# Optimization experiments

Hardware: AMD Instinct MI355X
Metric: run time of the kernel (lower is better)

The kernel has to match this reference:

```python
import jax, jax.numpy as jnp
import numpy as np

DEPTH, DIM, HEADS, DH = 6, 1024, 16, 64
INNER = int(DIM * 2 * 4 / 3)        # 2730 (GEGLU FFN inner dim)
INNER2 = INNER * 2                  # 5460
B, N = 2, 1024
NUM_BUCKETS, MAX_DIST = 32, 128
ALPHA = 0.1                         # grad_shrink alpha (identity in fwd)


def setup_inputs() -> dict:
    key = jax.random.key(0)
    ks = jax.random.split(key, 12)
    s = 0.02
    return {
        "x": jax.random.normal(ks[0], (B, N, DIM), jnp.float32),
        "rel_emb": jax.random.normal(ks[1], (NUM_BUCKETS, HEADS), jnp.float32) * s,
        "qn_g": jnp.ones((DEPTH, DIM), jnp.float32),
        "wq": jax.random.normal(ks[2], (DEPTH, DIM, HEADS * DH), jnp.float32) * s,
        "wkv": jax.random.normal(ks[3], (DEPTH, DIM, 2 * DH), jnp.float32) * s,
        "wo": jax.random.normal(ks[4], (DEPTH, HEADS * DH, DIM), jnp.float32) * s,
        "ln1_g": jnp.ones((DEPTH, DIM), jnp.float32),
        "w1": jax.random.normal(ks[5], (DEPTH, DIM, INNER2), jnp.float32) * s,
        "convw": jax.random.normal(ks[6], (DEPTH, INNER2, 3), jnp.float32) * s,
        "ln2_g": jnp.ones((DEPTH, INNER), jnp.float32),
        "w2": jax.random.normal(ks[7], (DEPTH, INNER, DIM), jnp.float32) * s,
        "final_g": jnp.ones((DIM,), jnp.float32),
    }


def _ln(x, g):
    m = jnp.mean(x, axis=-1, keepdims=True)
    v = jnp.mean(jnp.square(x - m), axis=-1, keepdims=True)
    return (x - m) * jax.lax.rsqrt(v + 1e-5) * g


def _rel_pos_bias(rel_emb, n):
    # T5-style buckets, causal variant (as in RelativePositionBias.forward)
    q_pos = jnp.arange(n)
    k_pos = jnp.arange(n)
    npos = jnp.maximum(q_pos[:, None] - k_pos[None, :], 0)   # -relative_position, clamped
    max_exact = NUM_BUCKETS // 2
    nf = jnp.maximum(npos, 1).astype(jnp.float32)
    val_large = max_exact + (jnp.log(nf / max_exact) / np.log(MAX_DIST / max_exact)
                             * (NUM_BUCKETS - max_exact)).astype(jnp.int32)
    val_large = jnp.minimum(val_large, NUM_BUCKETS - 1)
    bucket = jnp.where(npos < max_exact, npos, val_large)
    return rel_emb[bucket].transpose(2, 0, 1)  # [h, i, j]


def _forward(x, rel_emb, qn_g, wq, wkv, wo, ln1_g, w1, convw, ln2_g, w2, final_g):
    b, n, _ = x.shape
    x = x * ALPHA + jax.lax.stop_gradient(x) * (1.0 - ALPHA)  # grad_shrink
    bias = _rel_pos_bias(rel_emb, n)                          # [h, n, n]
    causal = jnp.triu(jnp.ones((n, n), bool), 1)
    neg = -jnp.finfo(x.dtype).max
    scale = DH ** -0.5

    for l in range(DEPTH):
        # --- causal self-attention (single-head K/V) ---
        h = _ln(x, qn_g[l])
        q = (h @ wq[l]).reshape(b, n, HEADS, DH).transpose(0, 2, 1, 3) * scale  # [b,h,n,d]
        kv = h @ wkv[l]
        k, v = kv[..., :DH], kv[..., DH:]                                       # [b,n,d]
        sim = jnp.einsum('bhid,bjd->bhij', q, k) + bias
        sim = jnp.where(causal, neg, sim)
        attn = jax.nn.softmax(sim, axis=-1)
        o = jnp.einsum('bhij,bjd->bhid', attn, v)
        o = o.transpose(0, 2, 1, 3).reshape(b, n, HEADS * DH)
        x = o @ wo[l] + x

        # --- FFN: LN -> Linear -> causal depthwise conv -> GEGLU -> LN -> Linear ---
        h = _ln(x, ln1_g[l]) @ w1[l]                 # [b, n, INNER2]
        hp = jnp.pad(h, ((0, 0), (2, 0), (0, 0)))    # causal pad
        w = convw[l]                                  # [INNER2, 3]
        h = hp[:, :-2] * w[:, 0] + hp[:, 1:-1] * w[:, 1] + hp[:, 2:] * w[:, 2]
        a, gate = h[..., :INNER], h[..., INNER:]
        h = jax.nn.gelu(gate, approximate=False) * a
        h = _ln(h, ln2_g[l]) @ w2[l]
        x = h + x

    return _ln(x, final_g)


def reference(x, rel_emb, qn_g, wq, wkv, wo, ln1_g, w1, convw, ln2_g, w2, final_g):
    return _forward(x, rel_emb, qn_g, wq, wkv, wo, ln1_g, w1, convw, ln2_g, w2, final_g)
```

## Files before the change

### kernel.cpp

```cpp
#include <hip/hip_runtime.h>
#include <math.h>

#define DEPTH 6
#define DIM 1024
#define HEADS 16
#define DH 64
#define INNER 2730
#define INNER2 5460
#define INNERP 2752
#define N1P 5504
#define BATCH 2
#define SEQ 1024
#define TOK (BATCH*SEQ)
#define QKVW 1152

#define OFF_WO 1179648ull
#define OFF_W1 2228224ull
#define OFF_W2 7864320ull
#define LWT    10682368ull
#define TILES_PER_LAYER 1312

typedef unsigned short ushort;
typedef __attribute__((ext_vector_type(8))) short short8;
typedef __attribute__((ext_vector_type(4))) short short4v;
typedef __attribute__((ext_vector_type(4))) unsigned short ushort4v;
typedef __attribute__((ext_vector_type(2))) unsigned short ushort2v;
typedef __attribute__((ext_vector_type(4))) float floatx4;

__device__ inline ushort f2bf(float f) {
  unsigned int u = __float_as_uint(f);
  u += 0x7FFF + ((u >> 16) & 1);
  return (ushort)(u >> 16);
}
__device__ inline float bf2f(ushort u) {
  return __uint_as_float(((unsigned int)u) << 16);
}

__device__ inline void gload_lds16(const ushort* g, ushort* l) {
  __builtin_amdgcn_global_load_lds(
      (const __attribute__((address_space(1))) unsigned int*)g,
      (__attribute__((address_space(3))) unsigned int*)l, 16, 0, 0);
}

__global__ void bias_frag_kernel(const float* __restrict__ rel_emb, float* __restrict__ bias_c) {
  int h = blockIdx.x >> 4, dq = blockIdx.x & 15;
  for (int i = threadIdx.x; i < 4096; i += 256) {
    int reg = i & 3, col = (i >> 2) & 15, j = (i >> 6) & 3, rowgrp = i >> 8;
    int row = rowgrp * 4 + reg, colg = j * 16 + col;
    int d = dq * 64 + row - colg;
    d = d < 0 ? 0 : (d > 1023 ? 1023 : d);
    int bucket;
    if (d < 16) {
      bucket = d;
    } else {
      float nf = (float)d;
      int vl = 16 + (int)(logf(nf / 16.0f) / 2.0794415416798357f * 16.0f);
      bucket = vl < 31 ? vl : 31;
    }
    bias_c[((size_t)(h * 16 + dq)) * 4096 + i] = rel_emb[bucket * HEADS + h];
  }
}

__device__ inline void transpose_body(const float* __restrict__ W, ushort* __restrict__ Wt,
                                      int K, int N, int Kp, int Np, float scale,
                                      int k0, int n0, size_t dst_row0) {
  __shared__ float t[64][65];
  int tid = threadIdx.x;
  int kl = tid >> 4, nc = (tid & 15) * 4;
#pragma unroll
  for (int it = 0; it < 4; it++) {
    int k = kl + it * 16;
    int gk = k0 + k, gn = n0 + nc;
    floatx4 v = {0.f, 0.f, 0.f, 0.f};
    if (gk < K && gn < N) v = *(const floatx4*)&W[(size_t)gk * N + gn];
    t[nc + 0][k] = v[0] * scale;
    t[nc + 1][k] = v[1] * scale;
    t[nc + 2][k] = v[2] * scale;
    t[nc + 3][k] = v[3] * scale;
  }
  __syncthreads();
  int nr = tid >> 3, q = tid & 7;
#pragma unroll
  for (int it = 0; it < 2; it++) {
    int n = nr + it * 32;
    if (n0 + n < Np) {
      short8 p;
#pragma unroll
      for (int e = 0; e < 8; e++) p[e] = (short)f2bf(t[n][q * 8 + e]);
      *(short8*)&Wt[(dst_row0 + n) * Kp + k0 + q * 8] = p;
    }
  }
}

__global__ __launch_bounds__(256) void transpose_vec(const float* __restrict__ W,
                                                     ushort* __restrict__ Wt,
                                                     int K, int N, int Kp, int Np, float scale) {
  transpose_body(W, Wt, K, N, Kp, Np, scale, blockIdx.y * 64, blockIdx.x * 64,
                 (size_t)blockIdx.x * 64);
}

__global__ __launch_bounds__(256) void transpose_qkv(const float* __restrict__ wq,
                                                     const float* __restrict__ wkv,
                                                     ushort* __restrict__ Wt) {
  int bx = blockIdx.x;
  if (bx < 16) {
    transpose_body(wq, Wt, 1024, 1024, 1024, 1024, 0.125f, blockIdx.y * 64, bx * 64,
                   (size_t)bx * 64);
  } else {
    transpose_body(wkv, Wt, 1024, 128, 1024, 128, 1.0f, blockIdx.y * 64, (bx - 16) * 64,
                   (size_t)1024 + (bx - 16) * 64);
  }
}

__device__ inline void transpose_body128(const float* __restrict__ W, ushort* __restrict__ Wt,
                                         int K, int N, int Kp, int Np, float scale,
                                         int k0, int n0, size_t dst_row0) {
  __shared__ float t[64][129];
  int tid = threadIdx.x;
  int kl = tid >> 4, nc = (tid & 15) * 4;
#pragma unroll
  for (int it = 0; it < 8; it++) {
    int k = kl + it * 16;
    int gk = k0 + k, gn = n0 + nc;
    floatx4 v = {0.f, 0.f, 0.f, 0.f};
    if (gk < K && gn < N) v = *(const floatx4*)&W[(size_t)gk * N + gn];
    t[nc + 0][k] = v[0] * scale;
    t[nc + 1][k] = v[1] * scale;
    t[nc + 2][k] = v[2] * scale;
    t[nc + 3][k] = v[3] * scale;
  }
  __syncthreads();
  int nr = tid >> 3, q = tid & 7;
#pragma unroll
  for (int p = 0; p < 2; p++) {
    int n = nr + p * 32;
    if (n0 + n < Np) {
      size_t rbase = (dst_row0 + n) * (size_t)Kp + k0;
#pragma unroll
      for (int it8 = 0; it8 < 2; it8++) {
        int k = it8 * 64 + q * 8;
        if (k0 + k < Kp) {
          short8 pk;
#pragma unroll
          for (int e = 0; e < 8; e++) pk[e] = (short)f2bf(t[n][k + e]);
          *(short8*)&Wt[rbase + k] = pk;
        }
      }
    }
  }
}

__global__ __launch_bounds__(256) void transpose_all(const float* __restrict__ wq,
                                                     const float* __restrict__ wkv,
                                                     const float* __restrict__ wo,
                                                     const float* __restrict__ w1,
                                                     const float* __restrict__ w2,
                                                     ushort* __restrict__ wtall) {
  int t = blockIdx.x;
  int l = t / TILES_PER_LAYER, r = t % TILES_PER_LAYER;
  ushort* base = wtall + (size_t)l * LWT;
  if (r < 144) {
    if (r < 128) {
      int bx = r & 15, by = r >> 4;
      transpose_body128(wq + (size_t)l * 1024 * 1024, base, 1024, 1024, 1024, 1024,
                        0.125f, by * 128, bx * 64, (size_t)bx * 64);
    } else {
      int q = r - 128, bx = q & 1, by = q >> 1;
      transpose_body128(wkv + (size_t)l * 1024 * 128, base, 1024, 128, 1024, 128,
                        1.0f, by * 128, bx * 64, 1024 + (size_t)bx * 64);
    }
  } else if (r < 272) {
    int q = r - 144, bx = q & 15, by = q >> 4;
    transpose_body128(wo + (size_t)l * 1024 * 1024, base + OFF_WO, 1024, 1024, 1024, 1024,
                      1.0f, by * 128, bx * 64, (size_t)bx * 64);
  } else if (r < 960) {
    int q = r - 272, bx = q % 86, by = q / 86;
    transpose_body128(w1 + (size_t)l * 1024 * 5460, base + OFF_W1, 1024, 5460, 1024, 5504,
                      1.0f, by * 128, bx * 64, (size_t)bx * 64);
  } else {
    int q = r - 960, bx = q & 15, by = q >> 4;
    transpose_body128(w2 + (size_t)l * 2730 * 1024, base + OFF_W2, 2730, 1024, 2752, 1024,
                      1.0f, by * 128, bx * 64, (size_t)bx * 64);
  }
}

template <typename OutT>
__global__ __launch_bounds__(256) void ln1024(const float* __restrict__ in,
                                              const float* __restrict__ g,
                                              OutT* __restrict__ out) {
  int row = blockIdx.x;
  int tid = threadIdx.x;
  floatx4 v = *(const floatx4*)&in[(size_t)row * 1024 + tid * 4];
  float s = v[0] + v[1] + v[2] + v[3];
  float ss = v[0] * v[0] + v[1] * v[1] + v[2] * v[2] + v[3] * v[3];
#pragma unroll
  for (int off = 32; off; off >>= 1) {
    s  += __shfl_down(s, off, 64);
    ss += __shfl_down(ss, off, 64);
  }
  __shared__ float l1[4], l2[4];
  int wid = tid >> 6, lane = tid & 63;
  if (lane == 0) { l1[wid] = s; l2[wid] = ss; }
  __syncthreads();
  if (tid == 0) {
    float a = l1[0] + l1[1] + l1[2] + l1[3];
    float bb = l2[0] + l2[1] + l2[2] + l2[3];
    float m = a * (1.0f / 1024.0f);
    float var = bb * (1.0f / 1024.0f) - m * m;
    l1[0] = m;
    l2[0] = rsqrtf(var + 1e-5f);
  }
  __syncthreads();
  float m = l1[0], r = l2[0];
  floatx4 gv = *(const floatx4*)&g[tid * 4];
  if constexpr (sizeof(OutT) == 2) {
    short4v p;
#pragma unroll
    for (int e = 0; e < 4; e++) p[e] = (short)f2bf((v[e] - m) * r * gv[e]);
    *(short4v*)&out[(size_t)row * 1024 + tid * 4] = p;
  } else {
    floatx4 p;
#pragma unroll
    for (int e = 0; e < 4; e++) p[e] = (v[e] - m) * r * gv[e];
    *(floatx4*)&out[(size_t)row * 1024 + tid * 4] = p;
  }
}

template <bool ADD, typename OutT>
__global__ __launch_bounds__(256) void gemm_mfma128(const ushort* __restrict__ A,
                                                    const ushort* __restrict__ Bt,
                                                    const float* __restrict__ Cin,
                                                    OutT* __restrict__ C,
                                                    int N, int K, float scale) {
  __shared__ ushort Als[128 * 64];
  __shared__ ushort Bls[128 * 64];
  int tid = threadIdx.x;
  int w = tid >> 6, lane = tid & 63;
  int wr = w >> 1, wc = w & 1;
  size_t row0 = (size_t)blockIdx.y * 128, col0 = (size_t)blockIdx.x * 128;

  const ushort* Ag = A + (row0 + w * 32 + (lane >> 3)) * (size_t)K + (lane & 7) * 8;
  const ushort* Bg = Bt + (col0 + w * 32 + (lane >> 3)) * (size_t)K + (lane & 7) * 8;
  ushort* Al = Als + w * 32 * 64;
  ushort* Bl = Bls + w * 32 * 64;

  floatx4 acc[4][4];
#pragma unroll
  for (int i = 0; i < 4; i++)
#pragma unroll
    for (int j = 0; j < 4; j++) { floatx4 z = {0.f, 0.f, 0.f, 0.f}; acc[i][j] = z; }

  int mrow = lane & 15, kq = (lane >> 4) * 8;
  for (int k0 = 0; k0 < K; k0 += 64) {
#pragma unroll
    for (int r = 0; r < 4; r++) {
      gload_lds16(Ag + (size_t)(r * 8) * K + k0, Al + r * 8 * 64);
      gload_lds16(Bg + (size_t)(r * 8) * K + k0, Bl + r * 8 * 64);
    }
    __syncthreads();
#pragma unroll
    for (int kk = 0; kk < 64; kk += 32) {
      short8 a[4], b[4];
#pragma unroll
      for (int i = 0; i < 4; i++)
        a[i] = *(const short8*)&Als[(wr * 64 + i * 16 + mrow) * 64 + kk + kq];
#pragma unroll
      for (int j = 0; j < 4; j++)
        b[j] = *(const short8*)&Bls[(wc * 64 + j * 16 + mrow) * 64 + kk + kq];
#pragma unroll
      for (int i = 0; i < 4; i++)
#pragma unroll
        for (int j = 0; j < 4; j++)
          acc[i][j] = __builtin_amdgcn_mfma_f32_16x16x32_bf16(a[i], b[j], acc[i][j], 0, 0, 0);
    }
    __syncthreads();
  }
  int orow = (lane >> 4) * 4, ocol = lane & 15;
#pragma unroll
  for (int i = 0; i < 4; i++) {
#pragma unroll
    for (int ii = 0; ii < 4; ii++) {
      size_t gr = row0 + wr * 64 + i * 16 + orow + ii;
#pragma unroll
      for (int j = 0; j < 4; j++) {
        size_t gc = col0 + wc * 64 + j * 16 + ocol;
        float v = acc[i][j][ii] * scale;
        if (ADD) v += Cin[gr * N + gc];
        if constexpr (sizeof(OutT) == 2) C[gr * N + gc] = f2bf(v);
        else C[gr * N + gc] = v;
      }
    }
  }
}

template <bool ADD, typename OutT>
__global__ __launch_bounds__(256) void gemm64x64(const ushort* __restrict__ A,
                                                 const ushort* __restrict__ Bt,
                                                 const float* __restrict__ Cin,
                                                 OutT* __restrict__ C,
                                                 int N, int K, float scale) {
  __shared__ ushort Als[64 * 64];
  __shared__ ushort Bls[64 * 64];
  int tid = threadIdx.x;
  int w = tid >> 6, lane = tid & 63;
  size_t row0 = (size_t)blockIdx.y * 64, col0 = (size_t)blockIdx.x * 64;

  const ushort* Ag = A + (row0 + (tid >> 3)) * (size_t)K + (tid & 7) * 8;
  const ushort* Bg = Bt + (col0 + (tid >> 3)) * (size_t)K + (tid & 7) * 8;
  ushort* Al = Als + (tid >> 3) * 64 + (tid & 7) * 8;
  ushort* Bl = Bls + (tid >> 3) * 64 + (tid & 7) * 8;

  floatx4 acc[4];
#pragma unroll
  for (int i = 0; i < 4; i++) { floatx4 z = {0.f, 0.f, 0.f, 0.f}; acc[i] = z; }

  int mrow = lane & 15, kq = (lane >> 4) * 8;
  for (int k0 = 0; k0 < K; k0 += 64) {
#pragma unroll
    for (int p = 0; p < 2; p++) {
      gload_lds16(Ag + (size_t)(p * 32) * K + k0, Al + p * 32 * 64);
      gload_lds16(Bg + (size_t)(p * 32) * K + k0, Bl + p * 32 * 64);
    }
    __syncthreads();
#pragma unroll
    for (int kk = 0; kk < 64; kk += 32) {
      short8 b = *(const short8*)&Bls[(w * 16 + mrow) * 64 + kk + kq];
#pragma unroll
      for (int i = 0; i < 4; i++) {
        short8 a = *(const short8*)&Als[(i * 16 + mrow) * 64 + kk + kq];
        acc[i] = __builtin_amdgcn_mfma_f32_16x16x32_bf16(a, b, acc[i], 0, 0, 0);
      }
    }
    __syncthreads();
  }
  int orow = (lane >> 4) * 4, ocol = lane & 15;
#pragma unroll
  for (int i = 0; i < 4; i++) {
#pragma unroll
    for (int ii = 0; ii < 4; ii++) {
      size_t gr = row0 + i * 16 + orow + ii;
      size_t gc = col0 + w * 16 + ocol;
      float v = acc[i][ii] * scale;
      if (ADD) v += Cin[gr * N + gc];
      if constexpr (sizeof(OutT) == 2) C[gr * N + gc] = f2bf(v);
      else C[gr * N + gc] = v;
    }
  }
}

__global__ __launch_bounds__(256) void convglu_ln(const ushort* __restrict__ h1,
                                                  const float* __restrict__ cw,
                                                  const float* __restrict__ lng,
                                                  ushort* __restrict__ out) {
  int t = blockIdx.x;
  int n = t & (SEQ - 1);
  int tid = threadIdx.x;
  const ushort* r0 = h1 + (size_t)t * N1P;
  float vals[3][4];
  float s = 0.f, ss = 0.f;
#pragma unroll
  for (int it = 0; it < 3; it++) {
    int c = (it * 256 + tid) * 4;
#pragma unroll
    for (int e = 0; e < 4; e++) vals[it][e] = 0.f;
    if (c < INNER) {
      ushort4v a2 = *(const ushort4v*)&r0[c];
      ushort4v a1 = {0, 0, 0, 0}, a0 = {0, 0, 0, 0};
      if (n >= 1) a1 = *(const ushort4v*)&r0[c - N1P];
      if (n >= 2) a0 = *(const ushort4v*)&r0[c - 2 * N1P];
      int cg = c + INNER;
      ushort2v g2a = *(const ushort2v*)&r0[cg];
      ushort2v g2b = *(const ushort2v*)&r0[cg + 2];
      ushort2v g1a = {0, 0}, g1b = {0, 0}, g0a = {0, 0}, g0b = {0, 0};
      if (n >= 1) { g1a = *(const ushort2v*)&r0[cg - N1P]; g1b = *(const ushort2v*)&r0[cg + 2 - N1P]; }
      if (n >= 2) { g0a = *(const ushort2v*)&r0[cg - 2 * N1P]; g0b = *(const ushort2v*)&r0[cg + 2 - 2 * N1P]; }
      const floatx4* cwa = (const floatx4*)(cw + (size_t)c * 3);
      floatx4 f0 = cwa[0], f1 = cwa[1], f2 = cwa[2];
      float wa[12] = {f0[0], f0[1], f0[2], f0[3], f1[0], f1[1], f1[2], f1[3],
                      f2[0], f2[1], f2[2], f2[3]};
#pragma unroll
      for (int e = 0; e < 4; e++) {
        int ce = c + e;
        if (ce < INNER) {
          float av = bf2f(a0[e]) * wa[e * 3] + bf2f(a1[e]) * wa[e * 3 + 1] +
                     bf2f(a2[e]) * wa[e * 3 + 2];
          int cge = ce + INNER;
          float w0g = cw[cge * 3], w1g = cw[cge * 3 + 1], w2g = cw[cge * 3 + 2];
          float g0f = bf2f(e < 2 ? g0a[e & 1] : g0b[e & 1]);
          float g1f = bf2f(e < 2 ? g1a[e & 1] : g1b[e & 1]);
          float g2f = bf2f(e < 2 ? g2a[e & 1] : g2b[e & 1]);
          float gvv = g0f * w0g + g1f * w1g + g2f * w2g;
          float gl = 0.5f * gvv * (1.0f + erff(gvv * 0.70710678118654752f));
          float val = gl * av;
          vals[it][e] = val;
          s += val;
          ss += val * val;
        }
      }
    }
  }
#pragma unroll
  for (int off = 32; off; off >>= 1) {
    s  += __shfl_down(s, off, 64);
    ss += __shfl_down(ss, off, 64);
  }
  __shared__ float l1[4], l2[4];
  int wid = tid >> 6, lane = tid & 63;
  if (lane == 0) { l1[wid] = s; l2[wid] = ss; }
  __syncthreads();
  if (tid == 0) {
    float a = l1[0] + l1[1] + l1[2] + l1[3];
    float bb = l2[0] + l2[1] + l2[2] + l2[3];
    float m = a * (1.0f / INNER);
    float var = bb * (1.0f / INNER) - m * m;
    l1[0] = m;
    l2[0] = rsqrtf(var + 1e-5f);
  }
  __syncthreads();
  float m = l1[0], r = l2[0];
#pragma unroll
  for (int it = 0; it < 3; it++) {
    int c = (it * 256 + tid) * 4;
    if (c < INNERP) {
      short4v p;
#pragma unroll
      for (int e = 0; e < 4; e++) {
        int ce = c + e;
        p[e] = (ce < INNER) ? (short)f2bf((vals[it][e] - m) * r * lng[ce]) : (short)0;
      }
      *(short4v*)&out[(size_t)t * INNERP + c] = p;
    }
  }
}

__global__ __launch_bounds__(256) void attn_mfma(const ushort* __restrict__ qkv,
                                                 const float* __restrict__ bias_c,
                                                 ushort* __restrict__ o) {
  __shared__ ushort Ks[64 * 72];
  __shared__ ushort Vt[64 * 72];
  __shared__ ushort Ps[64 * 72];
  __shared__ float arow[64];
  int tid = threadIdx.x;
  int lane = tid & 63, w = tid >> 6;
  int quad = lane >> 4, col = lane & 15;
  int b = blockIdx.x >> 4, h = blockIdx.x & 15;
  int y = blockIdx.y;
  int qt = (y < 8) ? (15 - y) : (y - 8);

  const ushort* qrow = qkv + (size_t)(b * SEQ + qt * 64 + w * 16 + col) * QKVW + h * 64;
  short8 qa[2];
  qa[0] = *(const short8*)&qrow[quad * 8];
  qa[1] = *(const short8*)&qrow[32 + quad * 8];

  float m_[4], l_[4];
  floatx4 oacc[4];
#pragma unroll
  for (int r = 0; r < 4; r++) { m_[r] = -1e30f; l_[r] = 0.f; }
#pragma unroll
  for (int mt = 0; mt < 4; mt++) { floatx4 z = {0.f, 0.f, 0.f, 0.f}; oacc[mt] = z; }

  for (int kc = 0; kc <= qt; kc++) {
    const ushort* kvb = qkv + (size_t)(b * SEQ + kc * 64) * QKVW;
#pragma unroll
    for (int it = 0; it < 2; it++) {
      int r = lane;
      int c8 = w + it * 4;
      short8 kk8 = *(const short8*)&kvb[(size_t)r * QKVW + 1024 + c8 * 8];
      *(short8*)&Ks[r * 72 + c8 * 8] = kk8;
      short8 vv = *(const short8*)&kvb[(size_t)r * QKVW + 1088 + c8 * 8];
#pragma unroll
      for (int e = 0; e < 8; e++) Vt[(c8 * 8 + e) * 72 + r] = (ushort)vv[e];
    }
    __syncthreads();

    floatx4 sarr[4];
#pragma unroll
    for (int j = 0; j < 4; j++) { floatx4 z = {0.f, 0.f, 0.f, 0.f}; sarr[j] = z; }
#pragma unroll
    for (int kk = 0; kk < 2; kk++) {
#pragma unroll
      for (int j = 0; j < 4; j++) {
        short8 kb = *(const short8*)&Ks[(j * 16 + col) * 72 + kk * 32 + quad * 8];
        sarr[j] = __builtin_amdgcn_mfma_f32_16x16x32_bf16(qa[kk], kb, sarr[j], 0, 0, 0);
      }
    }

    int dq = qt - kc;
    const floatx4* bc = (const floatx4*)(bias_c + ((size_t)(h * 16 + dq) * 4096 + (w * 4 + quad) * 256));
    float pv[4][4];
#pragma unroll
    for (int j = 0; j < 4; j++) {
      floatx4 bf = bc[j * 16 + col];
#pragma unroll
      for (int reg = 0; reg < 4; reg++) {
        float v = sarr[j][reg] + bf[reg];
        if (dq == 0 && (j * 16 + col) > (w * 16 + quad * 4 + reg)) v = -1e30f;
        pv[j][reg] = v;
      }
    }

#pragma unroll
    for (int reg = 0; reg < 4; reg++) {
      float cm = fmaxf(fmaxf(pv[0][reg], pv[1][reg]), fmaxf(pv[2][reg], pv[3][reg]));
      cm = fmaxf(cm, __shfl_xor(cm, 1, 64));
      cm = fmaxf(cm, __shfl_xor(cm, 2, 64));
      cm = fmaxf(cm, __shfl_xor(cm, 4, 64));
      cm = fmaxf(cm, __shfl_xor(cm, 8, 64));
      float nm = fmaxf(m_[reg], cm);
      float alpha = __expf(m_[reg] - nm);
      float rs = 0.f;
#pragma unroll
      for (int j = 0; j < 4; j++) {
        float e = __expf(pv[j][reg] - nm);
        pv[j][reg] = e;
        rs += e;
      }
      rs += __shfl_xor(rs, 1, 64);
      rs += __shfl_xor(rs, 2, 64);
      rs += __shfl_xor(rs, 4, 64);
      rs += __shfl_xor(rs, 8, 64);
      l_[reg] = l_[reg] * alpha + rs;
      m_[reg] = nm;
      if (col == 0) arow[w * 16 + quad * 4 + reg] = alpha;
    }

#pragma unroll
    for (int j = 0; j < 4; j++)
#pragma unroll
      for (int reg = 0; reg < 4; reg++)
        Ps[(w * 16 + quad * 4 + reg) * 72 + j * 16 + col] = f2bf(pv[j][reg]);

    asm volatile("s_waitcnt lgkmcnt(0)" ::: "memory");
    float aval = arow[w * 16 + col];
#pragma unroll
    for (int mt = 0; mt < 4; mt++) oacc[mt] *= aval;

#pragma unroll
    for (int kk = 0; kk < 2; kk++) {
      short8 pb = *(const short8*)&Ps[(w * 16 + col) * 72 + kk * 32 + quad * 8];
#pragma unroll
      for (int mt = 0; mt < 4; mt++) {
        short8 va = *(const short8*)&Vt[(mt * 16 + col) * 72 + kk * 32 + quad * 8];
        oacc[mt] = __builtin_amdgcn_mfma_f32_16x16x32_bf16(va, pb, oacc[mt], 0, 0, 0);
      }
    }
    __syncthreads();
  }

#pragma unroll
  for (int reg = 0; reg < 4; reg++)
    if (col == 0) arow[w * 16 + quad * 4 + reg] = 1.0f / l_[reg];
  asm volatile("s_waitcnt lgkmcnt(0)" ::: "memory");
  float lv = arow[w * 16 + col];
  size_t obase = (size_t)(b * SEQ + qt * 64 + w * 16 + col) * 1024 + h * 64;
#pragma unroll
  for (int mt = 0; mt < 4; mt++) {
    short4v pk;
#pragma unroll
    for (int reg = 0; reg < 4; reg++) pk[reg] = (short)f2bf(oacc[mt][reg] * lv);
    *(short4v*)&o[obase + mt * 16 + quad * 4] = pk;
  }
}

extern "C" void kernel_launch(void* const* d_in, const int* in_sizes, int n_in,
                              void* d_out, int out_size, void* d_ws, size_t ws_size,
                              hipStream_t stream) {
  const float* x_in    = (const float*)d_in[0];
  const float* rel_emb = (const float*)d_in[1];
  const float* qn_g    = (const float*)d_in[2];
  const float* wq      = (const float*)d_in[3];
  const float* wkv     = (const float*)d_in[4];
  const float* wo      = (const float*)d_in[5];
  const float* ln1_g   = (const float*)d_in[6];
  const float* w1      = (const float*)d_in[7];
  const float* convw   = (const float*)d_in[8];
  const float* ln2_g   = (const float*)d_in[9];
  const float* w2      = (const float*)d_in[10];
  const float* final_g = (const float*)d_in[11];
  float* out = (float*)d_out;

  float* xbuf   = (float*)d_ws;
  float* bias_c = xbuf + (size_t)TOK * DIM;
  ushort* hbuf  = (ushort*)(bias_c + (size_t)16 * 16 * 4096);
  ushort* obuf  = hbuf + (size_t)TOK * DIM;
  ushort* qkvbuf = obuf + (size_t)TOK * DIM;
  ushort* h1buf = qkvbuf + (size_t)TOK * QKVW;
  ushort* gbuf  = h1buf + (size_t)TOK * N1P;
  ushort* wtall = gbuf + (size_t)TOK * INNERP;

  size_t need = (size_t)((char*)(wtall + 6ull * LWT) - (char*)d_ws);
  bool big = ws_size >= need;

  bias_frag_kernel<<<256, 256, 0, stream>>>(rel_emb, bias_c);
  if (big)
    transpose_all<<<6 * TILES_PER_LAYER, 256, 0, stream>>>(wq, wkv, wo, w1, w2, wtall);

  for (int l = 0; l < DEPTH; l++) {
    const float* xres = (l == 0) ? x_in : xbuf;
    const ushort *wtq, *wto, *wt1, *wt2;
    if (big) {
      const ushort* bl = wtall + (size_t)l * LWT;
      wtq = bl; wto = bl + OFF_WO; wt1 = bl + OFF_W1; wt2 = bl + OFF_W2;
    } else {
      wtq = wto = wt1 = wt2 = wtall;
    }

    ln1024<ushort><<<TOK, 256, 0, stream>>>(xres, qn_g + l * DIM, hbuf);
    if (!big)
      transpose_qkv<<<dim3(18, 16), 256, 0, stream>>>(
          wq + (size_t)l * DIM * DIM, wkv + (size_t)l * DIM * 128, (ushort*)wtall);
    gemm64x64<false, ushort><<<dim3(18, 32), 256, 0, stream>>>(
        hbuf, wtq, nullptr, qkvbuf, QKVW, DIM, 1.0f);
    attn_mfma<<<dim3(BATCH * HEADS, 16), 256, 0, stream>>>(qkvbuf, bias_c, obuf);
    if (!big)
      transpose_vec<<<dim3(16, 16), 256, 0, stream>>>(
          wo + (size_t)l * DIM * DIM, (ushort*)wtall, DIM, DIM, DIM, DIM, 1.0f);
    gemm64x64<true, float><<<dim3(16, 32), 256, 0, stream>>>(
        obuf, wto, xres, xbuf, DIM, DIM, 1.0f);
    ln1024<ushort><<<TOK, 256, 0, stream>>>(xbuf, ln1_g + l * DIM, hbuf);
    if (!big)
      transpose_vec<<<dim3(86, 16), 256, 0, stream>>>(
          w1 + (size_t)l * DIM * INNER2, (ushort*)wtall, DIM, INNER2, DIM, N1P, 1.0f);
    gemm_mfma128<false, ushort><<<dim3(43, 16), 256, 0, stream>>>(
        hbuf, wt1, nullptr, h1buf, N1P, DIM, 1.0f);
    convglu_ln<<<TOK, 256, 0, stream>>>(
        h1buf, convw + (size_t)l * INNER2 * 3, ln2_g + l * INNER, gbuf);
    if (!big)
      transpose_vec<<<dim3(16, 43), 256, 0, stream>>>(
          w2 + (size_t)l * INNER * DIM, (ushort*)wtall, INNER, DIM, INNERP, DIM, 1.0f);
    gemm64x64<true, float><<<dim3(16, 32), 256, 0, stream>>>(
        gbuf, wt2, xbuf, xbuf, DIM, INNERP, 1.0f);
  }
  ln1024<float><<<TOK, 256, 0, stream>>>(xbuf, final_g, out);
}
```

Before: 1.635 ms.

## Double-buffer LDS tiles in both GEMM kernels with async prefetch

Both bf16 MFMA GEMM kernels now use two LDS buffers per operand. Each step issues the global-to-LDS loads for the next K tile before computing the current one, and waits with explicit vmcnt counts and raw barriers. This lets memory latency overlap with MFMA work instead of stalling at every K step. It doubles LDS use per block, which may reduce occupancy, and the correctness of the manual waitcnt depends on how the loads are counted.

```diff
diff --git a/kernel.cpp b/kernel.cpp
--- a/kernel.cpp
+++ b/kernel.cpp
@@ -19,6 +19,8 @@
 #define OFF_W2 7864320ull
 #define LWT    10682368ull
 #define TILES_PER_LAYER 1312
+
+#define VMCNT(n) asm volatile("s_waitcnt vmcnt(" #n ")" ::: "memory")
 
 typedef unsigned short ushort;
 typedef __attribute__((ext_vector_type(8))) short short8;
@@ -232,8 +234,8 @@
                                                     const float* __restrict__ Cin,
                                                     OutT* __restrict__ C,
                                                     int N, int K, float scale) {
-  __shared__ ushort Als[128 * 64];
-  __shared__ ushort Bls[128 * 64];
+  __shared__ ushort Als[2][128 * 64];
+  __shared__ ushort Bls[2][128 * 64];
   int tid = threadIdx.x;
   int w = tid >> 6, lane = tid & 63;
   int wr = w >> 1, wc = w & 1;
@@ -241,8 +243,7 @@
 
   const ushort* Ag = A + (row0 + w * 32 + (lane >> 3)) * (size_t)K + (lane & 7) * 8;
   const ushort* Bg = Bt + (col0 + w * 32 + (lane >> 3)) * (size_t)K + (lane & 7) * 8;
-  ushort* Al = Als + w * 32 * 64;
-  ushort* Bl = Bls + w * 32 * 64;
+  int wbase = w * 32 * 64;
 
   floatx4 acc[4][4];
 #pragma unroll
@@ -251,29 +252,46 @@
     for (int j = 0; j < 4; j++) { floatx4 z = {0.f, 0.f, 0.f, 0.f}; acc[i][j] = z; }
 
   int mrow = lane & 15, kq = (lane >> 4) * 8;
-  for (int k0 = 0; k0 < K; k0 += 64) {
-#pragma unroll
-    for (int r = 0; r < 4; r++) {
-      gload_lds16(Ag + (size_t)(r * 8) * K + k0, Al + r * 8 * 64);
-      gload_lds16(Bg + (size_t)(r * 8) * K + k0, Bl + r * 8 * 64);
-    }
-    __syncthreads();
+  int NT = K >> 6;
+
+#pragma unroll
+  for (int r = 0; r < 4; r++) {
+    gload_lds16(Ag + (size_t)(r * 8) * K, &Als[0][wbase + r * 8 * 64]);
+    gload_lds16(Bg + (size_t)(r * 8) * K, &Bls[0][wbase + r * 8 * 64]);
+  }
+
+  for (int t = 0; t < NT; t++) {
+    const ushort* Ac = Als[t & 1];
+    const ushort* Bc = Bls[t & 1];
+    if (t + 1 < NT) {
+      int nb = (t + 1) & 1;
+      int ko = (t + 1) << 6;
+#pragma unroll
+      for (int r = 0; r < 4; r++) {
+        gload_lds16(Ag + (size_t)(r * 8) * K + ko, &Als[nb][wbase + r * 8 * 64]);
+        gload_lds16(Bg + (size_t)(r * 8) * K + ko, &Bls[nb][wbase + r * 8 * 64]);
+      }
+      VMCNT(8);
+    } else {
+      VMCNT(0);
+    }
+    __builtin_amdgcn_s_barrier();
 #pragma unroll
     for (int kk = 0; kk < 64; kk += 32) {
       short8 a[4], b[4];
 #pragma unroll
       for (int i = 0; i < 4; i++)
-        a[i] = *(const short8*)&Als[(wr * 64 + i * 16 + mrow) * 64 + kk + kq];
+        a[i] = *(const short8*)&Ac[(wr * 64 + i * 16 + mrow) * 64 + kk + kq];
 #pragma unroll
       for (int j = 0; j < 4; j++)
-        b[j] = *(const short8*)&Bls[(wc * 64 + j * 16 + mrow) * 64 + kk + kq];
+        b[j] = *(const short8*)&Bc[(wc * 64 + j * 16 + mrow) * 64 + kk + kq];
 #pragma unroll
       for (int i = 0; i < 4; i++)
 #pragma unroll
         for (int j = 0; j < 4; j++)
           acc[i][j] = __builtin_amdgcn_mfma_f32_16x16x32_bf16(a[i], b[j], acc[i][j], 0, 0, 0);
     }
-    __syncthreads();
+    __builtin_amdgcn_s_barrier();
   }
   int orow = (lane >> 4) * 4, ocol = lane & 15;
 #pragma unroll
@@ -299,39 +317,53 @@
                                                  const float* __restrict__ Cin,
                                                  OutT* __restrict__ C,
                                                  int N, int K, float scale) {
-  __shared__ ushort Als[64 * 64];
-  __shared__ ushort Bls[64 * 64];
+  __shared__ ushort Als[2][64 * 64];
+  __shared__ ushort Bls[2][64 * 64];
   int tid = threadIdx.x;
   int w = tid >> 6, lane = tid & 63;
   size_t row0 = (size_t)blockIdx.y * 64, col0 = (size_t)blockIdx.x * 64;
 
   const ushort* Ag = A + (row0 + (tid >> 3)) * (size_t)K + (tid & 7) * 8;
   const ushort* Bg = Bt + (col0 + (tid >> 3)) * (size_t)K + (tid & 7) * 8;
-  ushort* Al = Als + (tid >> 3) * 64 + (tid & 7) * 8;
-  ushort* Bl = Bls + (tid >> 3) * 64 + (tid & 7) * 8;
+  int ldst = (tid >> 3) * 64 + (tid & 7) * 8;
 
   floatx4 acc[4];
 #pragma unroll
   for (int i = 0; i < 4; i++) { floatx4 z = {0.f, 0.f, 0.f, 0.f}; acc[i] = z; }
 
   int mrow = lane & 15, kq = (lane >> 4) * 8;
-  for (int k0 = 0; k0 < K; k0 += 64) {
-#pragma unroll
-    for (int p = 0; p < 2; p++) {
-      gload_lds16(Ag + (size_t)(p * 32) * K + k0, Al + p * 32 * 64);
-      gload_lds16(Bg + (size_t)(p * 32) * K + k0, Bl + p * 32 * 64);
-    }
-    __syncthreads();
+  int NT = K >> 6;
+
+  gload_lds16(Ag, &Als[0][ldst]);
+  gload_lds16(Ag + (size_t)32 * K, &Als[0][ldst + 2048]);
+  gload_lds16(Bg, &Bls[0][ldst]);
+  gload_lds16(Bg + (size_t)32 * K, &Bls[0][ldst + 2048]);
+
+  for (int t = 0; t < NT; t++) {
+    const ushort* Ac = Als[t & 1];
+    const ushort* Bc = Bls[t & 1];
+    if (t + 1 < NT) {
+      int nb = (t + 1) & 1;
+      int ko = (t + 1) << 6;
+      gload_lds16(Ag + ko, &Als[nb][ldst]);
+      gload_lds16(Ag + (size_t)32 * K + ko, &Als[nb][ldst + 2048]);
+      gload_lds16(Bg + ko, &Bls[nb][ldst]);
+      gload_lds16(Bg + (size_t)32 * K + ko, &Bls[nb][ldst + 2048]);
+      VMCNT(4);
+    } else {
+      VMCNT(0);
+    }
+    __builtin_amdgcn_s_barrier();
 #pragma unroll
     for (int kk = 0; kk < 64; kk += 32) {
-      short8 b = *(const short8*)&Bls[(w * 16 + mrow) * 64 + kk + kq];
+      short8 b = *(const short8*)&Bc[(w * 16 + mrow) * 64 + kk + kq];
 #pragma unroll
       for (int i = 0; i < 4; i++) {
-        short8 a = *(const short8*)&Als[(i * 16 + mrow) * 64 + kk + kq];
+        short8 a = *(const short8*)&Ac[(i * 16 + mrow) * 64 + kk + kq];
         acc[i] = __builtin_amdgcn_mfma_f32_16x16x32_bf16(a, b, acc[i], 0, 0, 0);
       }
     }
-    __syncthreads();
+    __builtin_amdgcn_s_barrier();
   }
   int orow = (lane >> 4) * 4, ocol = lane & 15;
 #pragma unroll
```

After: 1.553 ms. 5.0% less time.
